# Kernel tuning notes

Hardware: AMD Instinct MI355X
Metric: run time of the kernel (lower is better)

The kernel has to match this reference:

```python
import jax, jax.numpy as jnp
import numpy as np
import math

D_MODEL = 2048
D_QK = 128
D_V = 128
SEQ = 4096

def setup_inputs() -> dict:
    key = jax.random.key(0)
    ks = jax.random.split(key, 9)
    s = 1.0 / math.sqrt(D_MODEL)
    return {
        "input_q": jax.random.normal(ks[0], (SEQ, D_MODEL), jnp.float32),
        "input_k": jax.random.normal(ks[1], (SEQ, D_MODEL), jnp.float32),
        "input_v": jax.random.normal(ks[2], (SEQ, D_MODEL), jnp.float32),
        "WQ_w": jax.random.normal(ks[3], (D_QK, D_MODEL), jnp.float32) * s,
        "WQ_b": jax.random.normal(ks[4], (D_QK,), jnp.float32) * s,
        "WK_w": jax.random.normal(ks[5], (D_QK, D_MODEL), jnp.float32) * s,
        "WK_b": jax.random.normal(ks[6], (D_QK,), jnp.float32) * s,
        "WV_w": jax.random.normal(ks[7], (D_V, D_MODEL), jnp.float32) * s,
        "WV_b": jax.random.normal(ks[8], (D_V,), jnp.float32) * s,
    }

def reference(input_q, input_k, input_v, WQ_w, WQ_b, WK_w, WK_b, WV_w, WV_b):
    # Linear projections (torch nn.Linear: x @ W.T + b)
    Q = input_q @ WQ_w.T + WQ_b   # [S, d_qk]
    K = input_k @ WK_w.T + WK_b   # [S, d_qk]
    V = input_v @ WV_w.T + WV_b   # [S, d_v]
    S = Q.shape[0]
    # causal mask: -inf strictly above the diagonal, 0 elsewhere
    mask = jnp.triu(jnp.full((S, S), -jnp.inf, dtype=Q.dtype), k=1)
    # NOTE: original code adds mask BEFORE dividing by sqrt(d_model)
    scores = (Q @ K.T + mask) / math.sqrt(D_MODEL)  # [S, S]
    attn = jax.nn.softmax(scores, axis=-1)
    return attn @ V  # [S, d_v]
```

## Files before the change

kernel.cpp:

```cpp
#include <hip/hip_runtime.h>

#define SEQ 4096
#define DM  2048
#define DH  128

typedef __attribute__((ext_vector_type(8))) short bf16x8;
typedef __attribute__((ext_vector_type(4))) short short4v;
typedef __attribute__((ext_vector_type(4))) float f32x4;

__device__ inline short f2bf(float f) {
    union { float f; unsigned u; } x; x.f = f;
    unsigned r = x.u + 0x7fffu + ((x.u >> 16) & 1u);
    return (short)(r >> 16);
}

__device__ inline float fexp2(float f) { return __builtin_amdgcn_exp2f(f); }

__global__ __launch_bounds__(256) void convw_kernel(
    const float* __restrict__ wq, const float* __restrict__ wk, const float* __restrict__ wv,
    short* __restrict__ Wbf)
{
    int idx = blockIdx.x * 256 + threadIdx.x;
    int mat = idx >> 16;
    int off = (idx & 65535) * 4;
    const float* W = (mat == 0) ? wq : (mat == 1) ? wk : wv;
    float4 v = *reinterpret_cast<const float4*>(W + off);
    short4v s = { f2bf(v.x), f2bf(v.y), f2bf(v.z), f2bf(v.w) };
    *reinterpret_cast<short4v*>(Wbf + (size_t)mat * DH * DM + off) = s;
}

__global__ __launch_bounds__(256) void proj_kernel(
    const float* __restrict__ inq, const float* __restrict__ ink, const float* __restrict__ inv,
    const short* __restrict__ Wbf,
    const float* __restrict__ bq, const float* __restrict__ bk, const float* __restrict__ bv,
    float* __restrict__ Pqk, float* __restrict__ Pv)
{
    const int mat = blockIdx.y;
    const int s   = blockIdx.z;
    const float* A    = (mat == 0) ? inq : (mat == 1) ? ink : inv;
    const float* bias = (mat == 0) ? bq : (mat == 1) ? bk : bv;

    const int tid  = threadIdx.x;
    const int lane = tid & 63;
    const int w    = tid >> 6;
    const int g    = lane >> 4;
    const int c16  = lane & 15;
    const int i0   = blockIdx.x * 32;
    const int kb   = s * 1024;

    __shared__ short Alds[32][72];
    __shared__ short Wlds[128][72];

    const int ar = tid >> 3, ac = (tid & 7) * 8;
    const float* Aload = A + (size_t)(i0 + ar) * DM + kb + ac;
    const int wr = tid >> 1, wc = (tid & 1) * 32;
    const short* Wload = Wbf + (size_t)mat * DH * DM + (size_t)wr * DM + kb + wc;

    f32x4 acc[4];
    #pragma unroll
    for (int n = 0; n < 4; n++) acc[n] = (f32x4){0.f, 0.f, 0.f, 0.f};

    float4  abuf[4][2];
    bf16x8  wbuf[4][4];

    #pragma unroll
    for (int d = 0; d < 4; d++) {
        #pragma unroll
        for (int j = 0; j < 4; j++)
            wbuf[d][j] = *reinterpret_cast<const bf16x8*>(Wload + d * 64 + j * 8);
        abuf[d][0] = *reinterpret_cast<const float4*>(Aload + d * 64);
        abuf[d][1] = *reinterpret_cast<const float4*>(Aload + d * 64 + 4);
    }

    const int arow = (w >> 1) * 16 + c16;
    const int wbase = (w & 1) * 64;

    #pragma unroll
    for (int c = 0; c < 16; c++) {
        const int d = c & 3;
        {
            short4v s0 = { f2bf(abuf[d][0].x), f2bf(abuf[d][0].y),
                           f2bf(abuf[d][0].z), f2bf(abuf[d][0].w) };
            short4v s1 = { f2bf(abuf[d][1].x), f2bf(abuf[d][1].y),
                           f2bf(abuf[d][1].z), f2bf(abuf[d][1].w) };
            *reinterpret_cast<short4v*>(&Alds[ar][ac])     = s0;
            *reinterpret_cast<short4v*>(&Alds[ar][ac + 4]) = s1;
            #pragma unroll
            for (int j = 0; j < 4; j++)
                *reinterpret_cast<bf16x8*>(&Wlds[wr][wc + j * 8]) = wbuf[d][j];
        }
        if (c + 4 < 16) {
            #pragma unroll
            for (int j = 0; j < 4; j++)
                wbuf[d][j] = *reinterpret_cast<const bf16x8*>(Wload + (c + 4) * 64 + j * 8);
            abuf[d][0] = *reinterpret_cast<const float4*>(Aload + (c + 4) * 64);
            abuf[d][1] = *reinterpret_cast<const float4*>(Aload + (c + 4) * 64 + 4);
        }
        __syncthreads();
        #pragma unroll
        for (int kk = 0; kk < 2; kk++) {
            bf16x8 af = *reinterpret_cast<const bf16x8*>(&Alds[arow][kk * 32 + g * 8]);
            #pragma unroll
            for (int n = 0; n < 4; n++) {
                bf16x8 wf = *reinterpret_cast<const bf16x8*>(
                    &Wlds[wbase + n * 16 + c16][kk * 32 + g * 8]);
                acc[n] = __builtin_amdgcn_mfma_f32_16x16x32_bf16(af, wf, acc[n], 0, 0, 0);
            }
        }
        __syncthreads();
    }

    const int row0 = i0 + (w >> 1) * 16 + g * 4;
    if (mat < 2) {
        float* outp = Pqk + ((size_t)(mat * 2 + s) * SEQ) * DH;
        #pragma unroll
        for (int n = 0; n < 4; n++) {
            int col = wbase + n * 16 + c16;
            float b0 = (s == 0) ? bias[col] : 0.f;
            #pragma unroll
            for (int r = 0; r < 4; r++)
                outp[(size_t)(row0 + r) * DH + col] = acc[n][r] + b0;
        }
    } else {
        float* outp = Pv + (size_t)s * DH * SEQ;
        #pragma unroll
        for (int n = 0; n < 4; n++) {
            int col = wbase + n * 16 + c16;
            float b0 = (s == 0) ? bias[col] : 0.f;
            float4 f = { acc[n][0] + b0, acc[n][1] + b0, acc[n][2] + b0, acc[n][3] + b0 };
            *reinterpret_cast<float4*>(&outp[(size_t)col * SEQ + row0]) = f;
        }
    }
}

__global__ __launch_bounds__(256) void combine_kernel(
    const float* __restrict__ Pqk, const float* __restrict__ Pv,
    short* __restrict__ Qws, short* __restrict__ Kws, short* __restrict__ Vtws)
{
    const int b = blockIdx.x;
    if (b < 1024) {
        int tid = b * 256 + threadIdx.x;
        int mat = tid >> 17;
        int idx4 = (tid & 131071) * 4;
        const float* p0 = Pqk + ((size_t)(mat * 2 + 0) * SEQ) * DH;
        const float* p1 = Pqk + ((size_t)(mat * 2 + 1) * SEQ) * DH;
        float4 a = *reinterpret_cast<const float4*>(p0 + idx4);
        float4 c = *reinterpret_cast<const float4*>(p1 + idx4);
        short4v o = { f2bf(a.x + c.x), f2bf(a.y + c.y), f2bf(a.z + c.z), f2bf(a.w + c.w) };
        short* outp = (mat == 0) ? Qws : Kws;
        *reinterpret_cast<short4v*>(outp + idx4) = o;
    } else {
        int tid = (b - 1024) * 256 + threadIdx.x;
        int idx4 = tid * 4;
        float4 a = *reinterpret_cast<const float4*>(Pv + idx4);
        float4 c = *reinterpret_cast<const float4*>(Pv + (size_t)DH * SEQ + idx4);
        short4v o = { f2bf(a.x + c.x), f2bf(a.y + c.y), f2bf(a.z + c.z), f2bf(a.w + c.w) };
        *reinterpret_cast<short4v*>(Vtws + idx4) = o;
    }
}

__global__ __launch_bounds__(256) void flash_kernel(
    const short* __restrict__ Qws, const short* __restrict__ Kws, const short* __restrict__ Vtws,
    float* __restrict__ Opart, float* __restrict__ mpart, float* __restrict__ lpart)
{
    const int i  = blockIdx.x;
    const int w  = threadIdx.x >> 6;
    const int h  = blockIdx.y * 4 + w;
    const int NS = gridDim.y * 4;
    const int i0 = i * 16;
    const int lane = threadIdx.x & 63;
    const int g = lane >> 4, c16 = lane & 15;

    __shared__ short Slds[4][16][72];

    bf16x8 qf[4];
    #pragma unroll
    for (int kk = 0; kk < 4; kk++)
        qf[kk] = *reinterpret_cast<const bf16x8*>(Qws + (size_t)(i0 + c16) * DH + kk * 32 + g * 8);

    float m[4], lsum[4];
    f32x4 O[8];
    #pragma unroll
    for (int r = 0; r < 4; r++) { m[r] = -__builtin_inff(); lsum[r] = 0.f; }
    #pragma unroll
    for (int c = 0; c < 8; c++) O[c] = (f32x4){0.f, 0.f, 0.f, 0.f};

    const int njt = i / 4 + 1;
    const float C = 0.03188448666f;

    for (int jt = h; jt < njt; jt += NS) {
        const int j0 = jt * 64;
        f32x4 S[4];
        #pragma unroll
        for (int t = 0; t < 4; t++) S[t] = (f32x4){0.f, 0.f, 0.f, 0.f};
        #pragma unroll
        for (int kk = 0; kk < 4; kk++) {
            #pragma unroll
            for (int t = 0; t < 4; t++) {
                bf16x8 kf = *reinterpret_cast<const bf16x8*>(
                    Kws + (size_t)(j0 + t * 16 + c16) * DH + kk * 32 + g * 8);
                S[t] = __builtin_amdgcn_mfma_f32_16x16x32_bf16(qf[kk], kf, S[t], 0, 0, 0);
            }
        }
        float s2[4][4];
        #pragma unroll
        for (int t = 0; t < 4; t++) {
            int key = j0 + t * 16 + c16;
            #pragma unroll
            for (int r = 0; r < 4; r++) {
                int q = i0 + g * 4 + r;
                s2[t][r] = (key > q) ? -__builtin_inff() : S[t][r] * C;
            }
        }
        float mnew[4], alpha[4];
        #pragma unroll
        for (int r = 0; r < 4; r++) {
            float rm = fmaxf(fmaxf(s2[0][r], s2[1][r]), fmaxf(s2[2][r], s2[3][r]));
            rm = fmaxf(rm, __shfl_xor(rm, 1));
            rm = fmaxf(rm, __shfl_xor(rm, 2));
            rm = fmaxf(rm, __shfl_xor(rm, 4));
            rm = fmaxf(rm, __shfl_xor(rm, 8));
            mnew[r] = fmaxf(m[r], rm);
            alpha[r] = fexp2(m[r] - mnew[r]);
            m[r] = mnew[r];
        }
        #pragma unroll
        for (int r = 0; r < 4; r++) {
            float ps = 0.f;
            #pragma unroll
            for (int t = 0; t < 4; t++) {
                float p = fexp2(s2[t][r] - mnew[r]);
                ps += p;
                Slds[w][g * 4 + r][t * 16 + c16] = f2bf(p);
            }
            ps += __shfl_xor(ps, 1);
            ps += __shfl_xor(ps, 2);
            ps += __shfl_xor(ps, 4);
            ps += __shfl_xor(ps, 8);
            lsum[r] = lsum[r] * alpha[r] + ps;
            #pragma unroll
            for (int c = 0; c < 8; c++) O[c][r] *= alpha[r];
        }
        #pragma unroll
        for (int kk2 = 0; kk2 < 2; kk2++) {
            bf16x8 pf = *reinterpret_cast<const bf16x8*>(&Slds[w][c16][kk2 * 32 + g * 8]);
            #pragma unroll
            for (int c = 0; c < 8; c++) {
                bf16x8 vf = *reinterpret_cast<const bf16x8*>(
                    Vtws + (size_t)(c * 16 + c16) * SEQ + j0 + kk2 * 32 + g * 8);
                O[c] = __builtin_amdgcn_mfma_f32_16x16x32_bf16(pf, vf, O[c], 0, 0, 0);
            }
        }
    }
    #pragma unroll
    for (int c = 0; c < 8; c++) {
        int col = c * 16 + c16;
        #pragma unroll
        for (int r = 0; r < 4; r++)
            Opart[((size_t)h * SEQ + i0 + g * 4 + r) * DH + col] = O[c][r];
    }
    if (c16 == 0) {
        #pragma unroll
        for (int r = 0; r < 4; r++) {
            mpart[h * SEQ + i0 + g * 4 + r] = m[r];
            lpart[h * SEQ + i0 + g * 4 + r] = lsum[r];
        }
    }
}

__global__ __launch_bounds__(256) void merge_kernel(
    const float* __restrict__ Opart, const float* __restrict__ mpart, const float* __restrict__ lpart,
    float* __restrict__ out, int NS)
{
    const int row = blockIdx.x * 2 + (threadIdx.x >> 7);
    const int col = threadIdx.x & 127;
    float mh[16];
    float M = -__builtin_inff();
    for (int hh = 0; hh < NS; hh++) {
        mh[hh] = mpart[hh * SEQ + row];
        M = fmaxf(M, mh[hh]);
    }
    float denom = 0.f, num = 0.f;
    for (int hh = 0; hh < NS; hh++) {
        float wgt = fexp2(mh[hh] - M);
        denom += lpart[hh * SEQ + row] * wgt;
        num   += Opart[((size_t)hh * SEQ + row) * DH + col] * wgt;
    }
    out[(size_t)row * DH + col] = num / denom;
}

extern "C" void kernel_launch(void* const* d_in, const int* in_sizes, int n_in,
                              void* d_out, int out_size, void* d_ws, size_t ws_size,
                              hipStream_t stream) {
    const float* inq = (const float*)d_in[0];
    const float* ink = (const float*)d_in[1];
    const float* inv = (const float*)d_in[2];
    const float* wq  = (const float*)d_in[3];
    const float* bq  = (const float*)d_in[4];
    const float* wk  = (const float*)d_in[5];
    const float* bk  = (const float*)d_in[6];
    const float* wv  = (const float*)d_in[7];
    const float* bv  = (const float*)d_in[8];

    const int NS = 16;

    char* ws = (char*)d_ws;
    short* Qws   = (short*)(ws);
    short* Kws   = (short*)(ws + (1u << 20));
    short* Vtws  = (short*)(ws + (2u << 20));
    short* Wbf   = (short*)(ws + (3u << 20));
    float* Pqk   = (float*)(ws + 4718592);
    float* Pv    = (float*)(ws + 13107200);
    float* Opart = (float*)(ws + (3u << 20));
    float* mpart = (float*)(ws + (3u << 20) + (size_t)NS * SEQ * DH * 4);
    float* lpart = mpart + (size_t)NS * SEQ;

    convw_kernel<<<768, 256, 0, stream>>>(wq, wk, wv, Wbf);
    proj_kernel<<<dim3(128, 3, 2), 256, 0, stream>>>(inq, ink, inv, Wbf, bq, bk, bv, Pqk, Pv);
    combine_kernel<<<1536, 256, 0, stream>>>(Pqk, Pv, Qws, Kws, Vtws);
    flash_kernel<<<dim3(256, 4), 256, 0, stream>>>(Qws, Kws, Vtws, Opart, mpart, lpart);
    merge_kernel<<<2048, 256, 0, stream>>>(Opart, mpart, lpart, (float*)d_out, NS);
}
```

Before: 222.0 us.

## Share K/V tiles across waves via LDS with register prefetch in flash kernel

Each flash block now covers 64 query rows, one 16-row slice per wave. The 64-key K and V tiles are staged once into LDS and shared by all four waves, where before each wave fetched K and V straight from global memory. The next tile is prefetched into registers while the current one is computed, with barriers around the LDS swap. The key split drops from 16 to 8. This targets redundant global/L2 traffic, at the cost of extra LDS use, synchronisation, and coarser causal load balance across blocks.

```diff
diff --git a/kernel.cpp b/kernel.cpp
--- a/kernel.cpp
+++ b/kernel.cpp
@@ -3,6 +3,7 @@
 #define SEQ 4096
 #define DM  2048
 #define DH  128
+#define NSPLIT 8
 
 typedef __attribute__((ext_vector_type(8))) short bf16x8;
 typedef __attribute__((ext_vector_type(4))) short short4v;
@@ -163,15 +164,22 @@
     const short* __restrict__ Qws, const short* __restrict__ Kws, const short* __restrict__ Vtws,
     float* __restrict__ Opart, float* __restrict__ mpart, float* __restrict__ lpart)
 {
-    const int i  = blockIdx.x;
-    const int w  = threadIdx.x >> 6;
-    const int h  = blockIdx.y * 4 + w;
-    const int NS = gridDim.y * 4;
-    const int i0 = i * 16;
-    const int lane = threadIdx.x & 63;
+    const int qb = blockIdx.x;
+    const int y  = blockIdx.y;
+    const int tid = threadIdx.x;
+    const int w    = tid >> 6;
+    const int lane = tid & 63;
     const int g = lane >> 4, c16 = lane & 15;
-
+    const int i0 = qb * 64 + w * 16;
+
+    __shared__ short Klds[64][136];
+    __shared__ short Vlds[128][72];
     __shared__ short Slds[4][16][72];
+
+    const int kkey = tid >> 2,  kdim = (tid & 3) * 32;
+    const int vdim = tid >> 1,  vkey = (tid & 1) * 32;
+
+    bf16x8 kreg[4], vreg[4];
 
     bf16x8 qf[4];
     #pragma unroll
@@ -185,85 +193,123 @@
     #pragma unroll
     for (int c = 0; c < 8; c++) O[c] = (f32x4){0.f, 0.f, 0.f, 0.f};
 
-    const int njt = i / 4 + 1;
     const float C = 0.03188448666f;
 
-    for (int jt = h; jt < njt; jt += NS) {
-        const int j0 = jt * 64;
-        f32x4 S[4];
-        #pragma unroll
-        for (int t = 0; t < 4; t++) S[t] = (f32x4){0.f, 0.f, 0.f, 0.f};
-        #pragma unroll
-        for (int kk = 0; kk < 4; kk++) {
+    if (qb >= y) {
+        {
+            const int j0 = y * 64;
+            #pragma unroll
+            for (int j = 0; j < 4; j++) {
+                kreg[j] = *reinterpret_cast<const bf16x8*>(
+                    Kws + (size_t)(j0 + kkey) * DH + kdim + j * 8);
+                vreg[j] = *reinterpret_cast<const bf16x8*>(
+                    Vtws + (size_t)vdim * SEQ + j0 + vkey + j * 8);
+            }
+            #pragma unroll
+            for (int j = 0; j < 4; j++) {
+                *reinterpret_cast<bf16x8*>(&Klds[kkey][kdim + j * 8]) = kreg[j];
+                *reinterpret_cast<bf16x8*>(&Vlds[vdim][vkey + j * 8]) = vreg[j];
+            }
+        }
+        __syncthreads();
+
+        for (int jt = y; jt <= qb; jt += NSPLIT) {
+            const bool more = (jt + NSPLIT <= qb);
+            if (more) {
+                const int jn = (jt + NSPLIT) * 64;
+                #pragma unroll
+                for (int j = 0; j < 4; j++) {
+                    kreg[j] = *reinterpret_cast<const bf16x8*>(
+                        Kws + (size_t)(jn + kkey) * DH + kdim + j * 8);
+                    vreg[j] = *reinterpret_cast<const bf16x8*>(
+                        Vtws + (size_t)vdim * SEQ + jn + vkey + j * 8);
+                }
+            }
+            const int j0 = jt * 64;
+            f32x4 S[4];
+            #pragma unroll
+            for (int t = 0; t < 4; t++) S[t] = (f32x4){0.f, 0.f, 0.f, 0.f};
+            #pragma unroll
+            for (int kk = 0; kk < 4; kk++) {
+                #pragma unroll
+                for (int t = 0; t < 4; t++) {
+                    bf16x8 kf = *reinterpret_cast<const bf16x8*>(
+                        &Klds[t * 16 + c16][kk * 32 + g * 8]);
+                    S[t] = __builtin_amdgcn_mfma_f32_16x16x32_bf16(qf[kk], kf, S[t], 0, 0, 0);
+                }
+            }
+            float s2[4][4];
             #pragma unroll
             for (int t = 0; t < 4; t++) {
-                bf16x8 kf = *reinterpret_cast<const bf16x8*>(
-                    Kws + (size_t)(j0 + t * 16 + c16) * DH + kk * 32 + g * 8);
-                S[t] = __builtin_amdgcn_mfma_f32_16x16x32_bf16(qf[kk], kf, S[t], 0, 0, 0);
-            }
-        }
-        float s2[4][4];
-        #pragma unroll
-        for (int t = 0; t < 4; t++) {
-            int key = j0 + t * 16 + c16;
+                int key = j0 + t * 16 + c16;
+                #pragma unroll
+                for (int r = 0; r < 4; r++) {
+                    int q = i0 + g * 4 + r;
+                    s2[t][r] = (key > q) ? -__builtin_inff() : S[t][r] * C;
+                }
+            }
+            float mnew[4], alpha[4];
             #pragma unroll
             for (int r = 0; r < 4; r++) {
-                int q = i0 + g * 4 + r;
-                s2[t][r] = (key > q) ? -__builtin_inff() : S[t][r] * C;
-            }
-        }
-        float mnew[4], alpha[4];
+                float rm = fmaxf(fmaxf(s2[0][r], s2[1][r]), fmaxf(s2[2][r], s2[3][r]));
+                rm = fmaxf(rm, __shfl_xor(rm, 1));
+                rm = fmaxf(rm, __shfl_xor(rm, 2));
+                rm = fmaxf(rm, __shfl_xor(rm, 4));
+                rm = fmaxf(rm, __shfl_xor(rm, 8));
+                mnew[r] = fmaxf(m[r], rm);
+                alpha[r] = fexp2(m[r] - mnew[r]);
+                m[r] = mnew[r];
+            }
+            #pragma unroll
+            for (int r = 0; r < 4; r++) {
+                float ps = 0.f;
+                #pragma unroll
+                for (int t = 0; t < 4; t++) {
+                    float p = fexp2(s2[t][r] - mnew[r]);
+                    ps += p;
+                    Slds[w][g * 4 + r][t * 16 + c16] = f2bf(p);
+                }
+                ps += __shfl_xor(ps, 1);
+                ps += __shfl_xor(ps, 2);
+                ps += __shfl_xor(ps, 4);
+                ps += __shfl_xor(ps, 8);
+                lsum[r] = lsum[r] * alpha[r] + ps;
+                #pragma unroll
+                for (int c = 0; c < 8; c++) O[c][r] *= alpha[r];
+            }
+            #pragma unroll
+            for (int kk2 = 0; kk2 < 2; kk2++) {
+                bf16x8 pf = *reinterpret_cast<const bf16x8*>(&Slds[w][c16][kk2 * 32 + g * 8]);
+                #pragma unroll
+                for (int c = 0; c < 8; c++) {
+                    bf16x8 vf = *reinterpret_cast<const bf16x8*>(
+                        &Vlds[c * 16 + c16][kk2 * 32 + g * 8]);
+                    O[c] = __builtin_amdgcn_mfma_f32_16x16x32_bf16(pf, vf, O[c], 0, 0, 0);
+                }
+            }
+            __syncthreads();
+            if (more) {
+                #pragma unroll
+                for (int j = 0; j < 4; j++) {
+                    *reinterpret_cast<bf16x8*>(&Klds[kkey][kdim + j * 8]) = kreg[j];
+                    *reinterpret_cast<bf16x8*>(&Vlds[vdim][vkey + j * 8]) = vreg[j];
+                }
+                __syncthreads();
+            }
+        }
+        #pragma unroll
+        for (int c = 0; c < 8; c++) {
+            int col = c * 16 + c16;
+            #pragma unroll
+            for (int r = 0; r < 4; r++)
+                Opart[((size_t)y * SEQ + i0 + g * 4 + r) * DH + col] = O[c][r];
+        }
+    }
+    if (c16 == 0) {
         #pragma unroll
         for (int r = 0; r < 4; r++) {
-            float rm = fmaxf(fmaxf(s2[0][r], s2[1][r]), fmaxf(s2[2][r], s2[3][r]));
-            rm = fmaxf(rm, __shfl_xor(rm, 1));
-            rm = fmaxf(rm, __shfl_xor(rm, 2));
-            rm = fmaxf(rm, __shfl_xor(rm, 4));
-            rm = fmaxf(rm, __shfl_xor(rm, 8));
-            mnew[r] = fmaxf(m[r], rm);
-            alpha[r] = fexp2(m[r] - mnew[r]);
-            m[r] = mnew[r];
-        }
-        #pragma unroll
-        for (int r = 0; r < 4; r++) {
-            float ps = 0.f;
-            #pragma unroll
-            for (int t = 0; t < 4; t++) {
-                float p = fexp2(s2[t][r] - mnew[r]);
-                ps += p;
-                Slds[w][g * 4 + r][t * 16 + c16] = f2bf(p);
-            }
-            ps += __shfl_xor(ps, 1);
-            ps += __shfl_xor(ps, 2);
-            ps += __shfl_xor(ps, 4);
-            ps += __shfl_xor(ps, 8);
-            lsum[r] = lsum[r] * alpha[r] + ps;
-            #pragma unroll
-            for (int c = 0; c < 8; c++) O[c][r] *= alpha[r];
-        }
-        #pragma unroll
-        for (int kk2 = 0; kk2 < 2; kk2++) {
-            bf16x8 pf = *reinterpret_cast<const bf16x8*>(&Slds[w][c16][kk2 * 32 + g * 8]);
-            #pragma unroll
-            for (int c = 0; c < 8; c++) {
-                bf16x8 vf = *reinterpret_cast<const bf16x8*>(
-                    Vtws + (size_t)(c * 16 + c16) * SEQ + j0 + kk2 * 32 + g * 8);
-                O[c] = __builtin_amdgcn_mfma_f32_16x16x32_bf16(pf, vf, O[c], 0, 0, 0);
-            }
-        }
-    }
-    #pragma unroll
-    for (int c = 0; c < 8; c++) {
-        int col = c * 16 + c16;
-        #pragma unroll
-        for (int r = 0; r < 4; r++)
-            Opart[((size_t)h * SEQ + i0 + g * 4 + r) * DH + col] = O[c][r];
-    }
-    if (c16 == 0) {
-        #pragma unroll
-        for (int r = 0; r < 4; r++) {
-            mpart[h * SEQ + i0 + g * 4 + r] = m[r];
-            lpart[h * SEQ + i0 + g * 4 + r] = lsum[r];
+            mpart[y * SEQ + i0 + g * 4 + r] = m[r];
+            lpart[y * SEQ + i0 + g * 4 + r] = lsum[r];
         }
     }
 }
@@ -302,8 +348,6 @@
     const float* wv  = (const float*)d_in[7];
     const float* bv  = (const float*)d_in[8];
 
-    const int NS = 16;
-
     char* ws = (char*)d_ws;
     short* Qws   = (short*)(ws);
     short* Kws   = (short*)(ws + (1u << 20));
@@ -312,12 +356,12 @@
     float* Pqk   = (float*)(ws + 4718592);
     float* Pv    = (float*)(ws + 13107200);
     float* Opart = (float*)(ws + (3u << 20));
-    float* mpart = (float*)(ws + (3u << 20) + (size_t)NS * SEQ * DH * 4);
-    float* lpart = mpart + (size_t)NS * SEQ;
+    float* mpart = (float*)(ws + (3u << 20) + (size_t)NSPLIT * SEQ * DH * 4);
+    float* lpart = mpart + (size_t)NSPLIT * SEQ;
 
     convw_kernel<<<768, 256, 0, stream>>>(wq, wk, wv, Wbf);
     proj_kernel<<<dim3(128, 3, 2), 256, 0, stream>>>(inq, ink, inv, Wbf, bq, bk, bv, Pqk, Pv);
     combine_kernel<<<1536, 256, 0, stream>>>(Pqk, Pv, Qws, Kws, Vtws);
-    flash_kernel<<<dim3(256, 4), 256, 0, stream>>>(Qws, Kws, Vtws, Opart, mpart, lpart);
-    merge_kernel<<<2048, 256, 0, stream>>>(Opart, mpart, lpart, (float*)d_out, NS);
-}
+    flash_kernel<<<dim3(64, NSPLIT), 256, 0, stream>>>(Qws, Kws, Vtws, Opart, mpart, lpart);
+    merge_kernel<<<2048, 256, 0, stream>>>(Opart, mpart, lpart, (float*)d_out, NSPLIT);
+}
```

Measured after the change: 188.5 us. 1.18x faster.
